# Performance work log

Measured on AMD Instinct MI355X. Metric: run time of the kernel, lower is better.

Reference implementation:

```python
import jax, jax.numpy as jnp
import numpy as np

D = 2048   # dec_hidden_size == enc_hidden_size
IN = 512   # input_size
T = 4096   # T_enc


def setup_inputs() -> dict:
    key = jax.random.key(0)
    ks = jax.random.split(key, 20)
    s = 0.02
    zeros = jnp.zeros
    return {
        "data": jax.random.normal(ks[0], (1, IN), jnp.float32),
        "h0": jax.random.normal(ks[1], (1, 1, D), jnp.float32),
        "c0": jax.random.normal(ks[2], (1, 1, D), jnp.float32),
        "enc_output": jax.random.normal(ks[3], (T, 1, D), jnp.float32),
        "pi": jax.random.normal(ks[4], (T,), jnp.float32),
        "W_w": jax.random.normal(ks[5], (D, D), jnp.float32) * s,
        "U_w": jax.random.normal(ks[6], (D, D), jnp.float32) * s,
        "V_w": jax.random.normal(ks[7], (1, D), jnp.float32) * s,
        "lin_w": jax.random.normal(ks[8], (D, D), jnp.float32) * s,
        "lin_b": zeros((D,), jnp.float32),
        "lin1_w": jax.random.normal(ks[9], (D, D), jnp.float32) * s,
        "lin1_b": zeros((D,), jnp.float32),
        "lin2_w": jax.random.normal(ks[10], (D, D), jnp.float32) * s,
        "lin2_b": zeros((D,), jnp.float32),
        "dense_w": jax.random.normal(ks[11], (1, D), jnp.float32) * s,
        "dense_b": zeros((1,), jnp.float32),
        "W_ih": jax.random.normal(ks[12], (4 * D, IN + D), jnp.float32) * s,
        "W_hh": jax.random.normal(ks[13], (4 * D, D), jnp.float32) * s,
        "b_ih": zeros((4 * D,), jnp.float32),
        "b_hh": zeros((4 * D,), jnp.float32),
        "i": 100,
    }


def reference(data, h0, c0, enc_output, pi, W_w, U_w, V_w, lin_w, lin_b,
              lin1_w, lin1_b, lin2_w, lin2_b, dense_w, dense_b,
              W_ih, W_hh, b_ih, b_hh, i):
    Tl = pi.shape[0]
    output_pos = i + 1
    enc = enc_output[:, 0, :]                      # (T, E)
    # binary_vector(output_pos, T) @ pi : row k gets pi[output_pos+T-k-2] iff k >= output_pos-1
    k = jnp.arange(Tl)
    idx = output_pos + Tl - k - 2
    prod = jnp.where(k >= output_pos - 1, pi[jnp.clip(idx, 0, Tl - 1)], 0.0)
    u_h = (enc @ U_w.T) * prod[:, None]            # (T, D), per-channel scale by prod
    q = h0[0, 0] @ W_w.T                           # (D,)
    score = jnp.tanh(q[None, :] + u_h) @ V_w[0]    # (T,)
    score = jnp.where(k < output_pos, 0.0, score)  # attn_score[:j_null] = 0 (zero, not -inf)
    attn = jax.nn.softmax(score)                   # softmax over T
    context = attn @ enc                           # (E,)
    x = jnp.concatenate([context, data[0]])        # (E + IN,)
    # single-step LSTM, PyTorch gate order i,f,g,o
    gates = x @ W_ih.T + b_ih + h0[0, 0] @ W_hh.T + b_hh
    gi, gf, gg, go = jnp.split(gates, 4)
    c_new = jax.nn.sigmoid(gf) * c0[0, 0] + jax.nn.sigmoid(gi) * jnp.tanh(gg)
    h_new = jax.nn.sigmoid(go) * jnp.tanh(c_new)
    fc = h_new @ lin_w.T + lin_b
    l1 = fc @ lin1_w.T + lin1_b
    delta = jax.nn.softmax(l1)
    beta = jax.nn.softplus(fc @ lin2_w.T + lin2_b)
    gamma = l1 @ dense_w.T + dense_b               # original reuses linear1 for lin3
    return (gamma, beta, delta, h_new, c_new)
```

## Files before the change

kernel.cpp:

```cpp
#include <hip/hip_runtime.h>
#include <hip/hip_bf16.h>

#define D_  2048
#define IN_ 512
#define T_  4096
#define G4_ 8192

typedef __attribute__((ext_vector_type(4))) float f32x4;
typedef __attribute__((ext_vector_type(8))) short s16x8;
typedef unsigned short u16;

#define WS_PROD    0
#define WS_Q       (T_)
#define WS_X       (T_ + D_)
#define WS_PARTIAL (WS_X + D_ + IN_)
#define WS_ATTN    (WS_PARTIAL + T_*16)
#define WS_GATES   (WS_ATTN + T_)
#define WS_G2      (WS_GATES + G4_)
#define WS_FC      (WS_G2 + G4_)
#define WS_L1      (WS_FC + D_)
#define WS_HN      (WS_L1 + D_)
#define WS_BF16    (WS_HN + D_)
#define WS_FAST_BYTES ((size_t)WS_BF16 * 4 + ((size_t)T_ * D_ + (size_t)D_ * D_) * 2)

typedef const __attribute__((address_space(1))) void gas_t;
typedef __attribute__((address_space(3))) void las_t;

__device__ inline u16 bfbits(float f) {
  union { __hip_bfloat16 b; u16 s; } u; u.b = __float2bfloat16(f); return u.s;
}
__device__ inline float bf2f(u16 s) {
  union { unsigned u; float f; } v; v.u = ((unsigned)s) << 16; return v.f;
}

__device__ inline float wave_dot4(const float* __restrict__ w,
                                  const float* __restrict__ x, int n4, int lane) {
  float s = 0.f;
  const f32x4* w4 = (const f32x4*)w;
  const f32x4* x4 = (const f32x4*)x;
  for (int c = lane; c < n4; c += 64) {
    f32x4 a = w4[c], b = x4[c];
    s += a[0]*b[0] + a[1]*b[1] + a[2]*b[2] + a[3]*b[3];
  }
  #pragma unroll
  for (int m = 32; m >= 1; m >>= 1) s += __shfl_xor(s, m, 64);
  return s;
}

__global__ __launch_bounds__(256) void k_convert(const float* __restrict__ Ww,
    const float* __restrict__ h0, const float* __restrict__ pi,
    const float* __restrict__ data, const int* __restrict__ ip,
    const float* __restrict__ enc, const float* __restrict__ Uw,
    int do_convert, float* __restrict__ ws) {
  const int gidx = blockIdx.x * 256 + threadIdx.x;
  const int nth = 1024 * 256;
  if (do_convert) {
    u16* encB = (u16*)(ws + WS_BF16);
    u16* UwB  = encB + (size_t)T_ * D_;
    for (int c = gidx; c < (T_ * D_) / 8; c += nth) {
      const size_t base = (size_t)c * 8;
      f32x4 v0 = *(const f32x4*)(enc + base);
      f32x4 v1 = *(const f32x4*)(enc + base + 4);
      u16 t[8];
      #pragma unroll
      for (int e = 0; e < 4; ++e) { t[e] = bfbits(v0[e]); t[4 + e] = bfbits(v1[e]); }
      *(s16x8*)&encB[base] = *(s16x8*)&t[0];
    }
    for (int c = gidx; c < (D_ * D_) / 8; c += nth) {
      const size_t base = (size_t)c * 8;
      f32x4 v0 = *(const f32x4*)(Uw + base);
      f32x4 v1 = *(const f32x4*)(Uw + base + 4);
      u16 t[8];
      #pragma unroll
      for (int e = 0; e < 4; ++e) { t[e] = bfbits(v0[e]); t[4 + e] = bfbits(v1[e]); }
      *(s16x8*)&UwB[base] = *(s16x8*)&t[0];
    }
  }
  const int op = ip[0] + 1;
  if (gidx < T_) {
    float p = 0.f;
    if (gidx >= op - 1) {
      int idx = op + T_ - gidx - 2;
      idx = idx < 0 ? 0 : (idx > T_ - 1 ? T_ - 1 : idx);
      p = pi[idx];
    }
    ws[WS_PROD + gidx] = p;
  }
  if (gidx < D_) ws[WS_X + gidx] = 0.f;
  if (gidx < IN_) ws[WS_X + D_ + gidx] = data[gidx];
  const int gw = gidx >> 6, lane = gidx & 63;
  if (gw < D_) {
    float s = wave_dot4(Ww + (size_t)gw * D_, h0, D_ / 4, lane);
    if (lane == 0) ws[WS_Q + gw] = s;
  }
}

__global__ __launch_bounds__(512, 4) void k_gemm_bf16(
    const float* __restrict__ Vw, const float* __restrict__ h0,
    const float* __restrict__ Whh, float* __restrict__ ws) {
  __shared__ __align__(16) u16 Ah[2][128 * 64];
  __shared__ __align__(16) u16 Bh[2][128 * 64];
  const u16* encB = (const u16*)(ws + WS_BF16);
  const u16* UwB  = encB + (size_t)T_ * D_;
  const int tid = threadIdx.x, lane = tid & 63, wid = tid >> 6;
  const int wr = wid >> 2, wc = wid & 3;
  const int g = lane >> 4, lr = lane & 15;
  const int bid = blockIdx.x;
  const int wgid = (bid & 7) * 64 + (bid >> 3);
  const int mb = wgid >> 4, nb = wgid & 15;

  f32x4 acc[4][2];
  #pragma unroll
  for (int m = 0; m < 4; ++m)
    #pragma unroll
    for (int n = 0; n < 2; ++n) acc[m][n] = (f32x4){0.f, 0.f, 0.f, 0.f};

  const int c0 = tid,        r0 = c0 >> 3, s0 = (c0 & 7) ^ (r0 & 7);
  const int c1 = tid + 512,  r1 = c1 >> 3, s1 = (c1 & 7) ^ (r1 & 7);
  const u16* ga0 = encB + (size_t)(mb * 128 + r0) * D_ + s0 * 8;
  const u16* ga1 = encB + (size_t)(mb * 128 + r1) * D_ + s1 * 8;
  const u16* gb0 = UwB  + (size_t)(nb * 128 + r0) * D_ + s0 * 8;
  const u16* gb1 = UwB  + (size_t)(nb * 128 + r1) * D_ + s1 * 8;

  #define STAGE_(kt, b) do { \
    __builtin_amdgcn_global_load_lds((gas_t*)(ga0 + (kt) * 64), (las_t*)&Ah[b][c0 * 8], 16, 0, 0); \
    __builtin_amdgcn_global_load_lds((gas_t*)(ga1 + (kt) * 64), (las_t*)&Ah[b][c1 * 8], 16, 0, 0); \
    __builtin_amdgcn_global_load_lds((gas_t*)(gb0 + (kt) * 64), (las_t*)&Bh[b][c0 * 8], 16, 0, 0); \
    __builtin_amdgcn_global_load_lds((gas_t*)(gb1 + (kt) * 64), (las_t*)&Bh[b][c1 * 8], 16, 0, 0); \
  } while (0)

  STAGE_(0, 0);

  for (int ks = 0; ks < 32; ++ks) {
    const int cur = ks & 1;
    if (ks < 31) STAGE_(ks + 1, cur ^ 1);
    __builtin_amdgcn_sched_barrier(0);
    if (ks < 31) asm volatile("s_waitcnt vmcnt(4)" ::: "memory");
    else         asm volatile("s_waitcnt vmcnt(0)" ::: "memory");
    __builtin_amdgcn_sched_barrier(0);
    __builtin_amdgcn_s_barrier();
    #pragma unroll
    for (int kk = 0; kk < 2; ++kk) {
      const int koff = kk * 64 + g * 16;
      s16x8 af[4], bf[2];
      #pragma unroll
      for (int m = 0; m < 4; ++m) {
        const int r = wr * 64 + m * 16 + lr;
        af[m] = *(const s16x8*)((const char*)&Ah[cur][0] + r * 128 + (koff ^ ((r & 7) << 4)));
      }
      #pragma unroll
      for (int n = 0; n < 2; ++n) {
        const int r = wc * 32 + n * 16 + lr;
        bf[n] = *(const s16x8*)((const char*)&Bh[cur][0] + r * 128 + (koff ^ ((r & 7) << 4)));
      }
      #pragma unroll
      for (int m = 0; m < 4; ++m)
        #pragma unroll
        for (int n = 0; n < 2; ++n)
          acc[m][n] = __builtin_amdgcn_mfma_f32_16x16x32_bf16(af[m], bf[n], acc[m][n], 0, 0, 0);
    }
    __builtin_amdgcn_sched_barrier(0);
    asm volatile("s_waitcnt lgkmcnt(0)" ::: "memory");
    __builtin_amdgcn_sched_barrier(0);
    __builtin_amdgcn_s_barrier();
  }
  #undef STAGE_

  const float* q    = ws + WS_Q;
  const float* prod = ws + WS_PROD;
  float Vv[2], qv[2];
  #pragma unroll
  for (int n = 0; n < 2; ++n) {
    const int d = nb * 128 + wc * 32 + n * 16 + lr;
    Vv[n] = Vw[d]; qv[n] = q[d];
  }
  __syncthreads();
  float* red = (float*)&Ah[0][0];
  #pragma unroll
  for (int m = 0; m < 4; ++m) {
    #pragma unroll
    for (int r = 0; r < 4; ++r) {
      const int t_loc = wr * 64 + m * 16 + g * 4 + r;
      const float p = prod[mb * 128 + t_loc];
      float s = Vv[0] * tanhf(qv[0] + p * acc[m][0][r])
              + Vv[1] * tanhf(qv[1] + p * acc[m][1][r]);
      s += __shfl_xor(s, 1, 64);
      s += __shfl_xor(s, 2, 64);
      s += __shfl_xor(s, 4, 64);
      s += __shfl_xor(s, 8, 64);
      if (lr == 0) red[t_loc * 4 + wc] = s;
    }
  }
  __syncthreads();
  if (tid < 128) {
    const float s = red[tid * 4] + red[tid * 4 + 1] + red[tid * 4 + 2] + red[tid * 4 + 3];
    ws[WS_PARTIAL + (size_t)(mb * 128 + tid) * 16 + nb] = s;
  }

  const int rbase = bid * 16 + wid * 2;
  #pragma unroll
  for (int rr = 0; rr < 2; ++rr) {
    const int row = rbase + rr;
    float s = wave_dot4(Whh + (size_t)row * D_, h0, D_ / 4, lane);
    if (lane == 0) ws[WS_G2 + row] = s;
  }
}

__global__ __launch_bounds__(512, 4) void k_gemm_f32(
    const float* __restrict__ enc, const float* __restrict__ Uw,
    const float* __restrict__ Vw, const float* __restrict__ h0,
    const float* __restrict__ Whh, float* __restrict__ ws) {
  __shared__ __align__(16) u16 sbuf[2 * 128 * 40];
  u16* Ah = sbuf;
  u16* Bh = sbuf + 128 * 40;
  const int tid = threadIdx.x;
  const int lane = tid & 63, wid = tid >> 6;
  const int wr = wid >> 2, wc = wid & 3;
  const int g = lane >> 4, lr = lane & 15;
  const int mb = blockIdx.x, nb = blockIdx.y;

  f32x4 acc[4][2];
  #pragma unroll
  for (int m = 0; m < 4; ++m)
    #pragma unroll
    for (int n = 0; n < 2; ++n) acc[m][n] = (f32x4){0.f, 0.f, 0.f, 0.f};

  const int srow = tid >> 2;
  const int scol = (tid & 3) * 8;
  const float* pa0 = enc + (size_t)(mb * 128 + srow) * D_ + scol;
  const float* pb0 = Uw  + (size_t)(nb * 128 + srow) * D_ + scol;
  const int sidx = srow * 40 + scol;

  f32x4 an0 = *(const f32x4*)(pa0);
  f32x4 an1 = *(const f32x4*)(pa0 + 4);
  f32x4 bn0 = *(const f32x4*)(pb0);
  f32x4 bn1 = *(const f32x4*)(pb0 + 4);

  for (int ks = 0; ks < 64; ++ks) {
    f32x4 a0 = an0, a1 = an1, b0 = bn0, b1 = bn1;
    if (ks < 63) {
      an0 = *(const f32x4*)(pa0 + (ks + 1) * 32);
      an1 = *(const f32x4*)(pa0 + (ks + 1) * 32 + 4);
      bn0 = *(const f32x4*)(pb0 + (ks + 1) * 32);
      bn1 = *(const f32x4*)(pb0 + (ks + 1) * 32 + 4);
    }
    __syncthreads();
    __align__(16) u16 ah[8], bh[8];
    #pragma unroll
    for (int e = 0; e < 4; ++e) {
      ah[e] = bfbits(a0[e]); ah[4 + e] = bfbits(a1[e]);
      bh[e] = bfbits(b0[e]); bh[4 + e] = bfbits(b1[e]);
    }
    *(s16x8*)&Ah[sidx] = *(s16x8*)&ah[0];
    *(s16x8*)&Bh[sidx] = *(s16x8*)&bh[0];
    __syncthreads();

    s16x8 af[4], bf[2];
    #pragma unroll
    for (int m = 0; m < 4; ++m)
      af[m] = *(const s16x8*)&Ah[(wr * 64 + m * 16 + lr) * 40 + g * 8];
    #pragma unroll
    for (int n = 0; n < 2; ++n)
      bf[n] = *(const s16x8*)&Bh[(wc * 32 + n * 16 + lr) * 40 + g * 8];
    #pragma unroll
    for (int m = 0; m < 4; ++m)
      #pragma unroll
      for (int n = 0; n < 2; ++n)
        acc[m][n] = __builtin_amdgcn_mfma_f32_16x16x32_bf16(af[m], bf[n], acc[m][n], 0, 0, 0);
  }

  const float* q    = ws + WS_Q;
  const float* prod = ws + WS_PROD;
  float Vv[2], qv[2];
  #pragma unroll
  for (int n = 0; n < 2; ++n) {
    const int d = nb * 128 + wc * 32 + n * 16 + lr;
    Vv[n] = Vw[d]; qv[n] = q[d];
  }
  __syncthreads();
  float* red = (float*)sbuf;
  #pragma unroll
  for (int m = 0; m < 4; ++m) {
    #pragma unroll
    for (int r = 0; r < 4; ++r) {
      const int t_loc = wr * 64 + m * 16 + g * 4 + r;
      const float p = prod[mb * 128 + t_loc];
      float s = Vv[0] * tanhf(qv[0] + p * acc[m][0][r])
              + Vv[1] * tanhf(qv[1] + p * acc[m][1][r]);
      s += __shfl_xor(s, 1, 64);
      s += __shfl_xor(s, 2, 64);
      s += __shfl_xor(s, 4, 64);
      s += __shfl_xor(s, 8, 64);
      if (lr == 0) red[t_loc * 4 + wc] = s;
    }
  }
  __syncthreads();
  if (tid < 128) {
    const float s = red[tid * 4] + red[tid * 4 + 1] + red[tid * 4 + 2] + red[tid * 4 + 3];
    ws[WS_PARTIAL + (size_t)(mb * 128 + tid) * 16 + nb] = s;
  }
  const int flat = blockIdx.y * gridDim.x + blockIdx.x;
  const int rbase = flat * 16 + wid * 2;
  #pragma unroll
  for (int rr = 0; rr < 2; ++rr) {
    const int row = rbase + rr;
    float s = wave_dot4(Whh + (size_t)row * D_, h0, D_ / 4, lane);
    if (lane == 0) ws[WS_G2 + row] = s;
  }
}

__global__ __launch_bounds__(1024) void k_attn(const int* __restrict__ ip,
                                               float* __restrict__ ws) {
  __shared__ float sm[16];
  const int tid = threadIdx.x, lane = tid & 63, wid = tid >> 6;
  const int op = ip[0] + 1;
  float v[4];
  #pragma unroll
  for (int j = 0; j < 4; ++j) {
    const int t = tid + j * 1024;
    const f32x4* p = (const f32x4*)(ws + WS_PARTIAL + (size_t)t * 16);
    f32x4 p0 = p[0], p1 = p[1], p2 = p[2], p3 = p[3];
    float s = (p0[0]+p0[1]+p0[2]+p0[3]) + (p1[0]+p1[1]+p1[2]+p1[3])
            + (p2[0]+p2[1]+p2[2]+p2[3]) + (p3[0]+p3[1]+p3[2]+p3[3]);
    v[j] = (t < op) ? 0.f : s;
  }
  float mx = fmaxf(fmaxf(v[0], v[1]), fmaxf(v[2], v[3]));
  #pragma unroll
  for (int m = 32; m >= 1; m >>= 1) mx = fmaxf(mx, __shfl_xor(mx, m, 64));
  if (lane == 0) sm[wid] = mx;
  __syncthreads();
  if (tid == 0) {
    float m2 = sm[0];
    for (int w = 1; w < 16; ++w) m2 = fmaxf(m2, sm[w]);
    sm[0] = m2;
  }
  __syncthreads();
  mx = sm[0];
  __syncthreads();
  float e[4], ls = 0.f;
  #pragma unroll
  for (int j = 0; j < 4; ++j) { e[j] = expf(v[j] - mx); ls += e[j]; }
  #pragma unroll
  for (int m = 32; m >= 1; m >>= 1) ls += __shfl_xor(ls, m, 64);
  if (lane == 0) sm[wid] = ls;
  __syncthreads();
  if (tid == 0) {
    float s2 = 0.f;
    for (int w = 0; w < 16; ++w) s2 += sm[w];
    sm[0] = s2;
  }
  __syncthreads();
  const float inv = 1.f / sm[0];
  #pragma unroll
  for (int j = 0; j < 4; ++j) ws[WS_ATTN + tid + j * 1024] = e[j] * inv;
}

__global__ __launch_bounds__(256) void k_context_bf16(float* __restrict__ ws) {
  const u16* encB = (const u16*)(ws + WS_BF16);
  const int d = blockIdx.x * 256 + threadIdx.x;
  const int t0 = blockIdx.y * 256;
  const float* attn = ws + WS_ATTN;
  float s = 0.f;
  for (int t = t0; t < t0 + 256; ++t) s += attn[t] * bf2f(encB[(size_t)t * D_ + d]);
  atomicAdd(&ws[WS_X + d], s);
}
__global__ __launch_bounds__(256) void k_context_f32(const float* __restrict__ enc,
                                                     float* __restrict__ ws) {
  const int d = blockIdx.x * 256 + threadIdx.x;
  const int t0 = blockIdx.y * 256;
  const float* attn = ws + WS_ATTN;
  float s = 0.f;
  for (int t = t0; t < t0 + 256; ++t) s += attn[t] * enc[(size_t)t * D_ + d];
  atomicAdd(&ws[WS_X + d], s);
}

__global__ __launch_bounds__(256) void k_gates(const float* __restrict__ Wih,
    const float* __restrict__ bih, const float* __restrict__ bhh,
    float* __restrict__ ws) {
  const int wid = threadIdx.x >> 6, lane = threadIdx.x & 63;
  const int row = blockIdx.x * 4 + wid;
  float s = wave_dot4(Wih + (size_t)row * (D_ + IN_), ws + WS_X, (D_ + IN_) / 4, lane);
  if (lane == 0) ws[WS_GATES + row] = s + ws[WS_G2 + row] + bih[row] + bhh[row];
}

__global__ __launch_bounds__(256) void k_cell(const float* __restrict__ c0,
    float* __restrict__ ws, float* __restrict__ out) {
  const int d = blockIdx.x * 256 + threadIdx.x;
  const float* gt = ws + WS_GATES;
  const float gi = gt[d], gf = gt[D_ + d], gg = gt[2 * D_ + d], go = gt[3 * D_ + d];
  const float si = 1.f / (1.f + expf(-gi));
  const float sf = 1.f / (1.f + expf(-gf));
  const float so = 1.f / (1.f + expf(-go));
  const float cn = sf * c0[d] + si * tanhf(gg);
  const float hn = so * tanhf(cn);
  out[1 + 2 * D_ + d] = hn;
  out[1 + 3 * D_ + d] = cn;
  ws[WS_HN + d] = hn;
}

__global__ __launch_bounds__(256) void k_fc(const float* __restrict__ lw,
    const float* __restrict__ lb, float* __restrict__ ws) {
  const int wid = threadIdx.x >> 6, lane = threadIdx.x & 63;
  const int row = blockIdx.x * 4 + wid;
  float s = wave_dot4(lw + (size_t)row * D_, ws + WS_HN, D_ / 4, lane);
  if (lane == 0) ws[WS_FC + row] = s + lb[row];
}

__global__ __launch_bounds__(256) void k_l1beta(const float* __restrict__ l1w,
    const float* __restrict__ l1b, const float* __restrict__ l2w,
    const float* __restrict__ l2b, float* __restrict__ ws, float* __restrict__ out) {
  const int wid = threadIdx.x >> 6, lane = threadIdx.x & 63;
  const int row = blockIdx.x * 4 + wid;
  float a = wave_dot4(l1w + (size_t)row * D_, ws + WS_FC, D_ / 4, lane);
  float b = wave_dot4(l2w + (size_t)row * D_, ws + WS_FC, D_ / 4, lane);
  if (lane == 0) {
    ws[WS_L1 + row] = a + l1b[row];
    const float x = b + l2b[row];
    out[1 + row] = (x > 20.f) ? x : log1pf(expf(x));
  }
}

__global__ __launch_bounds__(256) void k_final(const float* __restrict__ dw,
    const float* __restrict__ db, float* __restrict__ ws, float* __restrict__ out) {
  __shared__ float sm[4];
  const int tid = threadIdx.x, lane = tid & 63, wid = tid >> 6;
  float v[8];
  #pragma unroll
  for (int j = 0; j < 8; ++j) v[j] = ws[WS_L1 + tid + j * 256];
  float mx = v[0];
  #pragma unroll
  for (int j = 1; j < 8; ++j) mx = fmaxf(mx, v[j]);
  #pragma unroll
  for (int m = 32; m >= 1; m >>= 1) mx = fmaxf(mx, __shfl_xor(mx, m, 64));
  if (lane == 0) sm[wid] = mx;
  __syncthreads();
  mx = fmaxf(fmaxf(sm[0], sm[1]), fmaxf(sm[2], sm[3]));
  __syncthreads();
  float e[8], ls = 0.f;
  #pragma unroll
  for (int j = 0; j < 8; ++j) { e[j] = expf(v[j] - mx); ls += e[j]; }
  #pragma unroll
  for (int m = 32; m >= 1; m >>= 1) ls += __shfl_xor(ls, m, 64);
  if (lane == 0) sm[wid] = ls;
  __syncthreads();
  ls = sm[0] + sm[1] + sm[2] + sm[3];
  __syncthreads();
  const float inv = 1.f / ls;
  float gp = 0.f;
  #pragma unroll
  for (int j = 0; j < 8; ++j) {
    out[1 + D_ + tid + j * 256] = e[j] * inv;
    gp += v[j] * dw[tid + j * 256];
  }
  #pragma unroll
  for (int m = 32; m >= 1; m >>= 1) gp += __shfl_xor(gp, m, 64);
  if (lane == 0) sm[wid] = gp;
  __syncthreads();
  if (tid == 0) out[0] = sm[0] + sm[1] + sm[2] + sm[3] + db[0];
}

extern "C" void kernel_launch(void* const* d_in, const int* in_sizes, int n_in,
                              void* d_out, int out_size, void* d_ws, size_t ws_size,
                              hipStream_t stream) {
  (void)in_sizes; (void)n_in; (void)out_size;
  const float* data   = (const float*)d_in[0];
  const float* h0     = (const float*)d_in[1];
  const float* c0     = (const float*)d_in[2];
  const float* enc    = (const float*)d_in[3];
  const float* pi     = (const float*)d_in[4];
  const float* Ww     = (const float*)d_in[5];
  const float* Uw     = (const float*)d_in[6];
  const float* Vw     = (const float*)d_in[7];
  const float* lin_w  = (const float*)d_in[8];
  const float* lin_b  = (const float*)d_in[9];
  const float* lin1_w = (const float*)d_in[10];
  const float* lin1_b = (const float*)d_in[11];
  const float* lin2_w = (const float*)d_in[12];
  const float* lin2_b = (const float*)d_in[13];
  const float* dw     = (const float*)d_in[14];
  const float* db     = (const float*)d_in[15];
  const float* Wih    = (const float*)d_in[16];
  const float* Whh    = (const float*)d_in[17];
  const float* bih    = (const float*)d_in[18];
  const float* bhh    = (const float*)d_in[19];
  const int*   ip     = (const int*)d_in[20];
  float* ws  = (float*)d_ws;
  float* out = (float*)d_out;
  const int fast = (ws_size >= WS_FAST_BYTES) ? 1 : 0;

  k_convert<<<1024, 256, 0, stream>>>(Ww, h0, pi, data, ip, enc, Uw, fast, ws);
  if (fast)
    k_gemm_bf16<<<512, 512, 0, stream>>>(Vw, h0, Whh, ws);
  else
    k_gemm_f32<<<dim3(T_ / 128, D_ / 128), 512, 0, stream>>>(enc, Uw, Vw, h0, Whh, ws);
  k_attn<<<1, 1024, 0, stream>>>(ip, ws);
  if (fast)
    k_context_bf16<<<dim3(D_ / 256, T_ / 256), 256, 0, stream>>>(ws);
  else
    k_context_f32<<<dim3(D_ / 256, T_ / 256), 256, 0, stream>>>(enc, ws);
  k_gates<<<G4_ / 4, 256, 0, stream>>>(Wih, bih, bhh, ws);
  k_cell<<<D_ / 256, 256, 0, stream>>>(c0, ws, out);
  k_fc<<<D_ / 4, 256, 0, stream>>>(lin_w, lin_b, ws);
  k_l1beta<<<D_ / 4, 256, 0, stream>>>(lin1_w, lin1_b, lin2_w, lin2_b, ws, out);
  k_final<<<1, 256, 0, stream>>>(dw, db, ws, out);
}
```

Measured before the change: 135.2 us.

## Use 4-wave blocks with 64x64 wave tiles and fold Whh GEMV into K-loop

The bf16 attention GEMM drops from 8 waves per 128x128 block to 4 waves, so each wave now computes a 64x64 tile. This raises MFMA work per LDS fragment load, at the cost of more accumulator registers and twice as many global-to-LDS loads per thread. The separate Whh·h0 GEMV tail, which streamed Whh after the GEMM finished, is now interleaved into the K loop: each thread loads a float4 slice of Whh and h0 per iteration and reduces across 16 lanes at the end. The goal is to hide that memory-bound GEMV behind the MFMA work. The wait count is adjusted to account for the extra loads.

```diff
diff --git a/kernel.cpp b/kernel.cpp
--- a/kernel.cpp
+++ b/kernel.cpp
@@ -95,7 +95,7 @@
   }
 }
 
-__global__ __launch_bounds__(512, 4) void k_gemm_bf16(
+__global__ __launch_bounds__(256, 2) void k_gemm_bf16(
     const float* __restrict__ Vw, const float* __restrict__ h0,
     const float* __restrict__ Whh, float* __restrict__ ws) {
   __shared__ __align__(16) u16 Ah[2][128 * 64];
@@ -103,78 +103,97 @@
   const u16* encB = (const u16*)(ws + WS_BF16);
   const u16* UwB  = encB + (size_t)T_ * D_;
   const int tid = threadIdx.x, lane = tid & 63, wid = tid >> 6;
-  const int wr = wid >> 2, wc = wid & 3;
+  const int wr = wid >> 1, wc = wid & 1;
   const int g = lane >> 4, lr = lane & 15;
   const int bid = blockIdx.x;
   const int wgid = (bid & 7) * 64 + (bid >> 3);
   const int mb = wgid >> 4, nb = wgid & 15;
 
-  f32x4 acc[4][2];
+  f32x4 acc[4][4];
   #pragma unroll
   for (int m = 0; m < 4; ++m)
     #pragma unroll
-    for (int n = 0; n < 2; ++n) acc[m][n] = (f32x4){0.f, 0.f, 0.f, 0.f};
-
-  const int c0 = tid,        r0 = c0 >> 3, s0 = (c0 & 7) ^ (r0 & 7);
-  const int c1 = tid + 512,  r1 = c1 >> 3, s1 = (c1 & 7) ^ (r1 & 7);
-  const u16* ga0 = encB + (size_t)(mb * 128 + r0) * D_ + s0 * 8;
-  const u16* ga1 = encB + (size_t)(mb * 128 + r1) * D_ + s1 * 8;
-  const u16* gb0 = UwB  + (size_t)(nb * 128 + r0) * D_ + s0 * 8;
-  const u16* gb1 = UwB  + (size_t)(nb * 128 + r1) * D_ + s1 * 8;
-
-  #define STAGE_(kt, b) do { \
-    __builtin_amdgcn_global_load_lds((gas_t*)(ga0 + (kt) * 64), (las_t*)&Ah[b][c0 * 8], 16, 0, 0); \
-    __builtin_amdgcn_global_load_lds((gas_t*)(ga1 + (kt) * 64), (las_t*)&Ah[b][c1 * 8], 16, 0, 0); \
-    __builtin_amdgcn_global_load_lds((gas_t*)(gb0 + (kt) * 64), (las_t*)&Bh[b][c0 * 8], 16, 0, 0); \
-    __builtin_amdgcn_global_load_lds((gas_t*)(gb1 + (kt) * 64), (las_t*)&Bh[b][c1 * 8], 16, 0, 0); \
-  } while (0)
-
-  STAGE_(0, 0);
+    for (int n = 0; n < 4; ++n) acc[m][n] = (f32x4){0.f, 0.f, 0.f, 0.f};
+
+  const u16* gA_[4]; const u16* gB_[4]; int lofs_[4];
+  #pragma unroll
+  for (int j = 0; j < 4; ++j) {
+    const int c = tid + j * 256;
+    const int r = c >> 3;
+    const int s = (c & 7) ^ (r & 7);
+    gA_[j] = encB + (size_t)(mb * 128 + r) * D_ + s * 8;
+    gB_[j] = UwB  + (size_t)(nb * 128 + r) * D_ + s * 8;
+    lofs_[j] = c * 8;
+  }
+  #define STAGE8(kt, b) do { \
+    _Pragma("unroll") \
+    for (int j_ = 0; j_ < 4; ++j_) { \
+      __builtin_amdgcn_global_load_lds((gas_t*)(gA_[j_] + (kt) * 64), (las_t*)&Ah[b][lofs_[j_]], 16, 0, 0); \
+      __builtin_amdgcn_global_load_lds((gas_t*)(gB_[j_] + (kt) * 64), (las_t*)&Bh[b][lofs_[j_]], 16, 0, 0); \
+    } } while (0)
+
+  const int hrow = tid >> 4, hcol = tid & 15;
+  const float* whp = Whh + (size_t)(bid * 16 + hrow) * D_ + hcol * 4;
+  const float* h0p = h0 + hcol * 4;
+  float whacc = 0.f;
+  f32x4 wv = *(const f32x4*)whp;
+  f32x4 hv = *(const f32x4*)h0p;
+
+  STAGE8(0, 0);
 
   for (int ks = 0; ks < 32; ++ks) {
     const int cur = ks & 1;
-    if (ks < 31) STAGE_(ks + 1, cur ^ 1);
+    const f32x4 wv_c = wv, hv_c = hv;
+    if (ks < 31) {
+      STAGE8(ks + 1, cur ^ 1);
+      wv = *(const f32x4*)(whp + (ks + 1) * 64);
+      hv = *(const f32x4*)(h0p + (ks + 1) * 64);
+    }
     __builtin_amdgcn_sched_barrier(0);
-    if (ks < 31) asm volatile("s_waitcnt vmcnt(4)" ::: "memory");
+    if (ks < 31) asm volatile("s_waitcnt vmcnt(10)" ::: "memory");
     else         asm volatile("s_waitcnt vmcnt(0)" ::: "memory");
     __builtin_amdgcn_sched_barrier(0);
     __builtin_amdgcn_s_barrier();
     #pragma unroll
     for (int kk = 0; kk < 2; ++kk) {
       const int koff = kk * 64 + g * 16;
-      s16x8 af[4], bf[2];
+      s16x8 af[4], bf[4];
       #pragma unroll
       for (int m = 0; m < 4; ++m) {
         const int r = wr * 64 + m * 16 + lr;
         af[m] = *(const s16x8*)((const char*)&Ah[cur][0] + r * 128 + (koff ^ ((r & 7) << 4)));
       }
       #pragma unroll
-      for (int n = 0; n < 2; ++n) {
-        const int r = wc * 32 + n * 16 + lr;
+      for (int n = 0; n < 4; ++n) {
+        const int r = wc * 64 + n * 16 + lr;
         bf[n] = *(const s16x8*)((const char*)&Bh[cur][0] + r * 128 + (koff ^ ((r & 7) << 4)));
       }
       #pragma unroll
       for (int m = 0; m < 4; ++m)
         #pragma unroll
-        for (int n = 0; n < 2; ++n)
+        for (int n = 0; n < 4; ++n)
           acc[m][n] = __builtin_amdgcn_mfma_f32_16x16x32_bf16(af[m], bf[n], acc[m][n], 0, 0, 0);
     }
+    whacc += wv_c[0]*hv_c[0] + wv_c[1]*hv_c[1] + wv_c[2]*hv_c[2] + wv_c[3]*hv_c[3];
     __builtin_amdgcn_sched_barrier(0);
     asm volatile("s_waitcnt lgkmcnt(0)" ::: "memory");
     __builtin_amdgcn_sched_barrier(0);
     __builtin_amdgcn_s_barrier();
   }
-  #undef STAGE_
+  #undef STAGE8
+
+  #pragma unroll
+  for (int m2 = 8; m2 >= 1; m2 >>= 1) whacc += __shfl_xor(whacc, m2, 64);
+  if (hcol == 0) ws[WS_G2 + bid * 16 + hrow] = whacc;
 
   const float* q    = ws + WS_Q;
   const float* prod = ws + WS_PROD;
-  float Vv[2], qv[2];
-  #pragma unroll
-  for (int n = 0; n < 2; ++n) {
-    const int d = nb * 128 + wc * 32 + n * 16 + lr;
+  float Vv[4], qv[4];
+  #pragma unroll
+  for (int n = 0; n < 4; ++n) {
+    const int d = nb * 128 + wc * 64 + n * 16 + lr;
     Vv[n] = Vw[d]; qv[n] = q[d];
   }
-  __syncthreads();
   float* red = (float*)&Ah[0][0];
   #pragma unroll
   for (int m = 0; m < 4; ++m) {
@@ -182,27 +201,20 @@
     for (int r = 0; r < 4; ++r) {
       const int t_loc = wr * 64 + m * 16 + g * 4 + r;
       const float p = prod[mb * 128 + t_loc];
-      float s = Vv[0] * tanhf(qv[0] + p * acc[m][0][r])
-              + Vv[1] * tanhf(qv[1] + p * acc[m][1][r]);
+      float s = 0.f;
+      #pragma unroll
+      for (int n = 0; n < 4; ++n) s += Vv[n] * tanhf(qv[n] + p * acc[m][n][r]);
       s += __shfl_xor(s, 1, 64);
       s += __shfl_xor(s, 2, 64);
       s += __shfl_xor(s, 4, 64);
       s += __shfl_xor(s, 8, 64);
-      if (lr == 0) red[t_loc * 4 + wc] = s;
+      if (lr == 0) red[t_loc * 2 + wc] = s;
     }
   }
   __syncthreads();
   if (tid < 128) {
-    const float s = red[tid * 4] + red[tid * 4 + 1] + red[tid * 4 + 2] + red[tid * 4 + 3];
+    const float s = red[tid * 2] + red[tid * 2 + 1];
     ws[WS_PARTIAL + (size_t)(mb * 128 + tid) * 16 + nb] = s;
-  }
-
-  const int rbase = bid * 16 + wid * 2;
-  #pragma unroll
-  for (int rr = 0; rr < 2; ++rr) {
-    const int row = rbase + rr;
-    float s = wave_dot4(Whh + (size_t)row * D_, h0, D_ / 4, lane);
-    if (lane == 0) ws[WS_G2 + row] = s;
   }
 }
 
@@ -490,7 +502,7 @@
 
   k_convert<<<1024, 256, 0, stream>>>(Ww, h0, pi, data, ip, enc, Uw, fast, ws);
   if (fast)
-    k_gemm_bf16<<<512, 512, 0, stream>>>(Vw, h0, Whh, ws);
+    k_gemm_bf16<<<512, 256, 0, stream>>>(Vw, h0, Whh, ws);
   else
     k_gemm_f32<<<dim3(T_ / 128, D_ / 128), 512, 0, stream>>>(enc, Uw, Vw, h0, Whh, ws);
   k_attn<<<1, 1024, 0, stream>>>(ip, ws);
```

After: 135.5 us. No clear change (+0.2%).

## Shrink bf16 GEMM tiles to 64x64 and split score reduction into parallel kernel

Applied to the files above, without the earlier changes.

The attention GEMM now uses 64x64 tiles with 256-thread blocks (2048 blocks instead of 512), which should fill the GPU better on this modest-sized problem at the cost of less operand reuse per tile. The W_hh row slice is prefetched into registers before the K loop so its latency overlaps the GEMM, and the per-row dot is done after. Partial scores now hold 32 column slices, and their reduction moves out of the single-block softmax kernel into a new multi-block k_score kernel. This adds one kernel launch but shortens the serial single-block phase.

```diff
diff --git a/kernel.cpp b/kernel.cpp
--- a/kernel.cpp
+++ b/kernel.cpp
@@ -14,7 +14,8 @@
 #define WS_Q       (T_)
 #define WS_X       (T_ + D_)
 #define WS_PARTIAL (WS_X + D_ + IN_)
-#define WS_ATTN    (WS_PARTIAL + T_*16)
+#define WS_SCORE   (WS_PARTIAL + T_*32)
+#define WS_ATTN    (WS_SCORE + T_)
 #define WS_GATES   (WS_ATTN + T_)
 #define WS_G2      (WS_GATES + G4_)
 #define WS_FC      (WS_G2 + G4_)
@@ -95,45 +96,52 @@
   }
 }
 
-__global__ __launch_bounds__(512, 4) void k_gemm_bf16(
+__global__ __launch_bounds__(256, 4) void k_gemm_bf16(
     const float* __restrict__ Vw, const float* __restrict__ h0,
     const float* __restrict__ Whh, float* __restrict__ ws) {
-  __shared__ __align__(16) u16 Ah[2][128 * 64];
-  __shared__ __align__(16) u16 Bh[2][128 * 64];
+  __shared__ __align__(16) u16 Ah[2][64 * 64];
+  __shared__ __align__(16) u16 Bh[2][64 * 64];
   const u16* encB = (const u16*)(ws + WS_BF16);
   const u16* UwB  = encB + (size_t)T_ * D_;
   const int tid = threadIdx.x, lane = tid & 63, wid = tid >> 6;
-  const int wr = wid >> 2, wc = wid & 3;
+  const int wr = wid >> 1, wc = wid & 1;
   const int g = lane >> 4, lr = lane & 15;
   const int bid = blockIdx.x;
-  const int wgid = (bid & 7) * 64 + (bid >> 3);
-  const int mb = wgid >> 4, nb = wgid & 15;
-
-  f32x4 acc[4][2];
-  #pragma unroll
-  for (int m = 0; m < 4; ++m)
+  const int wgid = (bid & 7) * 256 + (bid >> 3);
+  const int mb = wgid >> 5, nb = wgid & 31;
+
+  f32x4 acc[2][2];
+  #pragma unroll
+  for (int m = 0; m < 2; ++m)
     #pragma unroll
     for (int n = 0; n < 2; ++n) acc[m][n] = (f32x4){0.f, 0.f, 0.f, 0.f};
 
-  const int c0 = tid,        r0 = c0 >> 3, s0 = (c0 & 7) ^ (r0 & 7);
-  const int c1 = tid + 512,  r1 = c1 >> 3, s1 = (c1 & 7) ^ (r1 & 7);
-  const u16* ga0 = encB + (size_t)(mb * 128 + r0) * D_ + s0 * 8;
-  const u16* ga1 = encB + (size_t)(mb * 128 + r1) * D_ + s1 * 8;
-  const u16* gb0 = UwB  + (size_t)(nb * 128 + r0) * D_ + s0 * 8;
-  const u16* gb1 = UwB  + (size_t)(nb * 128 + r1) * D_ + s1 * 8;
-
-  #define STAGE_(kt, b) do { \
-    __builtin_amdgcn_global_load_lds((gas_t*)(ga0 + (kt) * 64), (las_t*)&Ah[b][c0 * 8], 16, 0, 0); \
-    __builtin_amdgcn_global_load_lds((gas_t*)(ga1 + (kt) * 64), (las_t*)&Ah[b][c1 * 8], 16, 0, 0); \
-    __builtin_amdgcn_global_load_lds((gas_t*)(gb0 + (kt) * 64), (las_t*)&Bh[b][c0 * 8], 16, 0, 0); \
-    __builtin_amdgcn_global_load_lds((gas_t*)(gb1 + (kt) * 64), (las_t*)&Bh[b][c1 * 8], 16, 0, 0); \
+  const int r0 = tid >> 3;
+  const int s0 = (tid & 7) ^ (r0 & 7);
+  const u16* gA0 = encB + (size_t)(mb * 64 + r0) * D_ + s0 * 8;
+  const u16* gA1 = encB + (size_t)(mb * 64 + r0 + 32) * D_ + s0 * 8;
+  const u16* gB0 = UwB  + (size_t)(nb * 64 + r0) * D_ + s0 * 8;
+  const u16* gB1 = UwB  + (size_t)(nb * 64 + r0 + 32) * D_ + s0 * 8;
+  const int lo0 = tid * 8, lo1 = (tid + 256) * 8;
+
+  #define STAGE4(kt, b) do { \
+    __builtin_amdgcn_global_load_lds((gas_t*)(gA0 + (kt) * 64), (las_t*)&Ah[b][lo0], 16, 0, 0); \
+    __builtin_amdgcn_global_load_lds((gas_t*)(gA1 + (kt) * 64), (las_t*)&Ah[b][lo1], 16, 0, 0); \
+    __builtin_amdgcn_global_load_lds((gas_t*)(gB0 + (kt) * 64), (las_t*)&Bh[b][lo0], 16, 0, 0); \
+    __builtin_amdgcn_global_load_lds((gas_t*)(gB1 + (kt) * 64), (las_t*)&Bh[b][lo1], 16, 0, 0); \
   } while (0)
 
-  STAGE_(0, 0);
+  const int hrow = bid * 4 + wid;
+  const float* whp = Whh + (size_t)hrow * D_ + lane * 4;
+  f32x4 wv[8];
+  #pragma unroll
+  for (int j = 0; j < 8; ++j) wv[j] = *(const f32x4*)(whp + j * 256);
+
+  STAGE4(0, 0);
 
   for (int ks = 0; ks < 32; ++ks) {
     const int cur = ks & 1;
-    if (ks < 31) STAGE_(ks + 1, cur ^ 1);
+    if (ks < 31) STAGE4(ks + 1, cur ^ 1);
     __builtin_amdgcn_sched_barrier(0);
     if (ks < 31) asm volatile("s_waitcnt vmcnt(4)" ::: "memory");
     else         asm volatile("s_waitcnt vmcnt(0)" ::: "memory");
@@ -142,10 +150,10 @@
     #pragma unroll
     for (int kk = 0; kk < 2; ++kk) {
       const int koff = kk * 64 + g * 16;
-      s16x8 af[4], bf[2];
+      s16x8 af[2], bf[2];
       #pragma unroll
-      for (int m = 0; m < 4; ++m) {
-        const int r = wr * 64 + m * 16 + lr;
+      for (int m = 0; m < 2; ++m) {
+        const int r = wr * 32 + m * 16 + lr;
         af[m] = *(const s16x8*)((const char*)&Ah[cur][0] + r * 128 + (koff ^ ((r & 7) << 4)));
       }
       #pragma unroll
@@ -154,7 +162,7 @@
         bf[n] = *(const s16x8*)((const char*)&Bh[cur][0] + r * 128 + (koff ^ ((r & 7) << 4)));
       }
       #pragma unroll
-      for (int m = 0; m < 4; ++m)
+      for (int m = 0; m < 2; ++m)
         #pragma unroll
         for (int n = 0; n < 2; ++n)
           acc[m][n] = __builtin_amdgcn_mfma_f32_16x16x32_bf16(af[m], bf[n], acc[m][n], 0, 0, 0);
@@ -164,45 +172,49 @@
     __builtin_amdgcn_sched_barrier(0);
     __builtin_amdgcn_s_barrier();
   }
-  #undef STAGE_
+  #undef STAGE4
+
+  {
+    const float* h0p = h0 + lane * 4;
+    float whacc = 0.f;
+    #pragma unroll
+    for (int j = 0; j < 8; ++j) {
+      f32x4 hv = *(const f32x4*)(h0p + j * 256);
+      whacc += wv[j][0]*hv[0] + wv[j][1]*hv[1] + wv[j][2]*hv[2] + wv[j][3]*hv[3];
+    }
+    #pragma unroll
+    for (int m2 = 32; m2 >= 1; m2 >>= 1) whacc += __shfl_xor(whacc, m2, 64);
+    if (lane == 0) ws[WS_G2 + hrow] = whacc;
+  }
 
   const float* q    = ws + WS_Q;
   const float* prod = ws + WS_PROD;
   float Vv[2], qv[2];
   #pragma unroll
   for (int n = 0; n < 2; ++n) {
-    const int d = nb * 128 + wc * 32 + n * 16 + lr;
+    const int d = nb * 64 + wc * 32 + n * 16 + lr;
     Vv[n] = Vw[d]; qv[n] = q[d];
   }
-  __syncthreads();
   float* red = (float*)&Ah[0][0];
   #pragma unroll
-  for (int m = 0; m < 4; ++m) {
+  for (int m = 0; m < 2; ++m) {
     #pragma unroll
     for (int r = 0; r < 4; ++r) {
-      const int t_loc = wr * 64 + m * 16 + g * 4 + r;
-      const float p = prod[mb * 128 + t_loc];
+      const int t_loc = wr * 32 + m * 16 + g * 4 + r;
+      const float p = prod[mb * 64 + t_loc];
       float s = Vv[0] * tanhf(qv[0] + p * acc[m][0][r])
               + Vv[1] * tanhf(qv[1] + p * acc[m][1][r]);
       s += __shfl_xor(s, 1, 64);
       s += __shfl_xor(s, 2, 64);
       s += __shfl_xor(s, 4, 64);
       s += __shfl_xor(s, 8, 64);
-      if (lr == 0) red[t_loc * 4 + wc] = s;
-    }
-  }
-  __syncthreads();
-  if (tid < 128) {
-    const float s = red[tid * 4] + red[tid * 4 + 1] + red[tid * 4 + 2] + red[tid * 4 + 3];
-    ws[WS_PARTIAL + (size_t)(mb * 128 + tid) * 16 + nb] = s;
-  }
-
-  const int rbase = bid * 16 + wid * 2;
-  #pragma unroll
-  for (int rr = 0; rr < 2; ++rr) {
-    const int row = rbase + rr;
-    float s = wave_dot4(Whh + (size_t)row * D_, h0, D_ / 4, lane);
-    if (lane == 0) ws[WS_G2 + row] = s;
+      if (lr == 0) red[t_loc * 2 + wc] = s;
+    }
+  }
+  __syncthreads();
+  if (tid < 64) {
+    const float s = red[tid * 2] + red[tid * 2 + 1];
+    ws[WS_PARTIAL + (size_t)(mb * 64 + tid) * 32 + nb] = s;
   }
 }
 
@@ -297,7 +309,8 @@
   __syncthreads();
   if (tid < 128) {
     const float s = red[tid * 4] + red[tid * 4 + 1] + red[tid * 4 + 2] + red[tid * 4 + 3];
-    ws[WS_PARTIAL + (size_t)(mb * 128 + tid) * 16 + nb] = s;
+    ws[WS_PARTIAL + (size_t)(mb * 128 + tid) * 32 + nb] = s;
+    ws[WS_PARTIAL + (size_t)(mb * 128 + tid) * 32 + nb + 16] = 0.f;
   }
   const int flat = blockIdx.y * gridDim.x + blockIdx.x;
   const int rbase = flat * 16 + wid * 2;
@@ -309,21 +322,26 @@
   }
 }
 
-__global__ __launch_bounds__(1024) void k_attn(const int* __restrict__ ip,
+__global__ __launch_bounds__(256) void k_score(const int* __restrict__ ip,
                                                float* __restrict__ ws) {
+  const int t = blockIdx.x * 256 + threadIdx.x;
+  const int op = ip[0] + 1;
+  const f32x4* p = (const f32x4*)(ws + WS_PARTIAL + (size_t)t * 32);
+  float s = 0.f;
+  #pragma unroll
+  for (int c = 0; c < 8; ++c) {
+    f32x4 v = p[c];
+    s += v[0] + v[1] + v[2] + v[3];
+  }
+  ws[WS_SCORE + t] = (t < op) ? 0.f : s;
+}
+
+__global__ __launch_bounds__(1024) void k_attn(float* __restrict__ ws) {
   __shared__ float sm[16];
   const int tid = threadIdx.x, lane = tid & 63, wid = tid >> 6;
-  const int op = ip[0] + 1;
   float v[4];
   #pragma unroll
-  for (int j = 0; j < 4; ++j) {
-    const int t = tid + j * 1024;
-    const f32x4* p = (const f32x4*)(ws + WS_PARTIAL + (size_t)t * 16);
-    f32x4 p0 = p[0], p1 = p[1], p2 = p[2], p3 = p[3];
-    float s = (p0[0]+p0[1]+p0[2]+p0[3]) + (p1[0]+p1[1]+p1[2]+p1[3])
-            + (p2[0]+p2[1]+p2[2]+p2[3]) + (p3[0]+p3[1]+p3[2]+p3[3]);
-    v[j] = (t < op) ? 0.f : s;
-  }
+  for (int j = 0; j < 4; ++j) v[j] = ws[WS_SCORE + tid + j * 1024];
   float mx = fmaxf(fmaxf(v[0], v[1]), fmaxf(v[2], v[3]));
   #pragma unroll
   for (int m = 32; m >= 1; m >>= 1) mx = fmaxf(mx, __shfl_xor(mx, m, 64));
@@ -490,10 +508,11 @@
 
   k_convert<<<1024, 256, 0, stream>>>(Ww, h0, pi, data, ip, enc, Uw, fast, ws);
   if (fast)
-    k_gemm_bf16<<<512, 512, 0, stream>>>(Vw, h0, Whh, ws);
+    k_gemm_bf16<<<2048, 256, 0, stream>>>(Vw, h0, Whh, ws);
   else
     k_gemm_f32<<<dim3(T_ / 128, D_ / 128), 512, 0, stream>>>(enc, Uw, Vw, h0, Whh, ws);
-  k_attn<<<1, 1024, 0, stream>>>(ip, ws);
+  k_score<<<T_ / 256, 256, 0, stream>>>(ip, ws);
+  k_attn<<<1, 1024, 0, stream>>>(ws);
   if (fast)
     k_context_bf16<<<dim3(D_ / 256, T_ / 256), 256, 0, stream>>>(ws);
   else
```

After: 146.9 us. +8.6%, slower.
